# Kernel optimization log

Measured on AMD Instinct MI355X. Metric: run time of the kernel, lower is better.

The kernel has to match this reference:

```python
import jax, jax.numpy as jnp
import numpy as np
from jax import lax

H_IMG, W_IMG = 1280, 1280
STRIDES = (8, 16, 32, 64, 128)
FEAT_SHAPES = tuple((H_IMG // s) * (W_IMG // s) for s in STRIDES)  # (25600,6400,1600,400,100)
N_POINTS = sum(FEAT_SHAPES)  # 34100
NUM_CLASSES = 1
TOPK = 1000
SCORE_THRESH = 0.05
NMS_THRESH = 0.5
MAX_DET = 300
BATCH = 8
N_GT = 200


def make_points():
    # matches AnchorFreePS.reference_points: cell centers at stride*i + stride//2, (cx, cy) order
    pts = []
    for s in STRIDES:
        h, w = H_IMG // s, W_IMG // s
        cx = np.arange(w, dtype=np.float32) * s + s // 2
        cy = np.arange(h, dtype=np.float32) * s + s // 2
        gy, gx = np.meshgrid(cy, cx, indexing='ij')
        pts.append(np.stack([gx, gy], axis=-1).reshape(-1, 2))
    return jnp.asarray(np.concatenate(pts, axis=0))


def setup_inputs() -> dict:
    key = jax.random.key(0)
    k1, k2, k3, k4 = jax.random.split(key, 4)
    points = make_points()  # [N,2]
    xy = jax.random.uniform(k1, (BATCH, N_GT, 2), minval=0.0, maxval=1000.0)
    wh = jax.random.uniform(k2, (BATCH, N_GT, 2), minval=20.0, maxval=260.0)
    gt_boxes = jnp.concatenate([xy, xy + wh], axis=-1)  # [B,M,4] x1y1x2y2
    cls_logits = jax.random.normal(k3, (BATCH, N_POINTS, NUM_CLASSES)) * 1.5 - 3.0
    regression = jax.random.uniform(k4, (BATCH, N_POINTS, 4)) * 0.1  # normalized ltrb codes
    return {"points": points, "gt_boxes": gt_boxes, "cls_logits": cls_logits, "regression": regression}


def match_points_to_boxes(points, gt_boxes):
    # point-in-box test + area-cost argmin (compute_loss matched_idxs)
    px = points[None, :, None, 0]  # [1,N,1]
    py = points[None, :, None, 1]
    b = gt_boxes[:, None, :, :]    # [B,1,M,4]
    inside = (px >= b[..., 0]) & (px <= b[..., 2]) & (py >= b[..., 1]) & (py <= b[..., 3])  # [B,N,M]
    matched = jnp.any(inside, axis=-1)  # [B,N]
    areas = (gt_boxes[..., 2] - gt_boxes[..., 0]) * (gt_boxes[..., 3] - gt_boxes[..., 1])  # [B,M]
    BIG = jnp.float32(2 ** 31 - 1)  # torch.iinfo(torch.int).max
    cost = jnp.where(inside, areas[:, None, :], BIG)
    idx = jnp.argmin(cost, axis=-1)
    return jnp.where(matched, idx, -1)


def decode_boxes(rel, pts):
    # FCOSBoxCoder.decode_single with weights (1,1,1,1)
    l = rel[:, 0] * W_IMG
    t = rel[:, 1] * H_IMG
    r = rel[:, 2] * W_IMG
    b = rel[:, 3] * H_IMG
    x, y = pts[:, 0], pts[:, 1]
    return jnp.stack([x - l, y - t, x + r, y + b], axis=-1)


def clip_boxes(boxes):
    return jnp.stack([
        jnp.clip(boxes[:, 0], 0.0, W_IMG),
        jnp.clip(boxes[:, 1], 0.0, H_IMG),
        jnp.clip(boxes[:, 2], 0.0, W_IMG),
        jnp.clip(boxes[:, 3], 0.0, H_IMG)], axis=-1)


def nms(boxes, scores, labels, valid_init):
    # fixed-size sequential NMS equivalent to batched_nms (same-label suppression)
    work = lax.stop_gradient(jnp.where(valid_init, scores, -jnp.inf))

    def body(w, _):
        i = jnp.argmax(w)
        s = w[i]
        box = boxes[i]
        x1 = jnp.maximum(box[0], boxes[:, 0])
        y1 = jnp.maximum(box[1], boxes[:, 1])
        x2 = jnp.minimum(box[2], boxes[:, 2])
        y2 = jnp.minimum(box[3], boxes[:, 3])
        inter = jnp.clip(x2 - x1, 0.0) * jnp.clip(y2 - y1, 0.0)
        a1 = (box[2] - box[0]) * (box[3] - box[1])
        a2 = (boxes[:, 2] - boxes[:, 0]) * (boxes[:, 3] - boxes[:, 1])
        iou = inter / (a1 + a2 - inter + 1e-9)
        supp = (iou > NMS_THRESH) & (labels == labels[i])
        w = jnp.where(supp, -jnp.inf, w).at[i].set(-jnp.inf)
        return w, (i, s)

    _, (idxs, picked) = lax.scan(body, work, None, length=MAX_DET)
    valid = picked > -jnp.inf
    return idxs, valid


def postprocess_image(points, cls_i, reg_i):
    bx_list, sc_list, lb_list = [], [], []
    off = 0
    for size in FEAT_SHAPES:  # fixed small level loop
        sl = slice(off, off + size)
        off += size
        scores = jax.nn.sigmoid(cls_i[sl]).reshape(-1)  # [size*C]
        k = min(TOPK, size * NUM_CLASSES)
        sc, idx = lax.top_k(scores, k)
        a = idx // NUM_CLASSES
        lb = idx % NUM_CLASSES
        bx = clip_boxes(decode_boxes(reg_i[sl][a], points[sl][a]))
        bx_list.append(bx)
        sc_list.append(sc)
        lb_list.append(lb)
    boxes = jnp.concatenate(bx_list, axis=0)
    scores = jnp.concatenate(sc_list, axis=0)
    labels = jnp.concatenate(lb_list, axis=0)
    idxs, valid = nms(boxes, scores, labels, scores > SCORE_THRESH)
    out_boxes = jnp.where(valid[:, None], boxes[idxs], 0.0)
    out_scores = jnp.where(valid, scores[idxs], 0.0)
    out_labels = jnp.where(valid, labels[idxs], -1)
    return out_boxes, out_scores, out_labels, valid


def reference(points, gt_boxes, cls_logits, regression):
    matched_idxs = match_points_to_boxes(points, gt_boxes)  # [B,N]
    boxes, scores, labels, valid = jax.vmap(
        lambda c, r: postprocess_image(points, c, r))(cls_logits, regression)
    return matched_idxs, boxes, scores, labels, valid
```

## Files before the change

kernel.cpp:

```cpp
#include <hip/hip_runtime.h>
#include <stdint.h>

#define N_POINTS   34100
#define BATCH      8
#define N_GT       200
#define NLEV       5
#define NCAND      3500
#define MAX_DET    300
#define SCORE_TH   0.05f
#define NMS_TH     0.5f
#define IMG        1280.0f
#define NBIN       4096
#define TIE_CAP    4096
#define MTH 0.50000002980232238769531250

#define OUT_MATCH  0
#define OUT_BOXES  272800
#define OUT_SCORES 282400
#define OUT_LABELS 284800
#define OUT_VALID  287200

#define WS_KEYS    0
#define WS_SBOX    2632192
#define WS_SSC     3080192
#define WS_MASK    3192192
#define WS_DIAG    9500032
#define MASK_STRIDE 98560
#define DIAG_STRIDE 3520

typedef unsigned long long u64;
typedef uint32_t u32;

__device__ __forceinline__ int mask_off(int c) {
    int g = c >> 6;
    return 64 * (55 * g - (g * (g - 1)) / 2) + (c - (g << 6)) * (55 - g);
}

__device__ __forceinline__ int level_of(int p) {
    return (p < 25600) ? 0 : (p < 32000) ? 1 : (p < 33600) ? 2 : (p < 34000) ? 3 : 4;
}
__device__ __forceinline__ int loff_of(int l) {
    return (l == 0) ? 0 : (l == 1) ? 25600 : (l == 2) ? 32000 : (l == 3) ? 33600 : 34000;
}
__device__ __forceinline__ int k_of(int l) {
    return (l == 0) ? 1000 : (l == 1) ? 1000 : (l == 2) ? 1000 : (l == 3) ? 400 : 100;
}
__device__ __forceinline__ u64 readlane64(u64 v, int t) {
    u32 lo = (u32)__builtin_amdgcn_readlane((int)(u32)v, t);
    u32 hi = (u32)__builtin_amdgcn_readlane((int)(u32)(v >> 32), t);
    return ((u64)hi << 32) | lo;
}

#define MPT 2
__global__ __launch_bounds__(256)
void match_key_kernel(const float* __restrict__ points,
                      const float* __restrict__ gt,
                      const float* __restrict__ logits,
                      float* __restrict__ out_match,
                      u32* __restrict__ keys) {
#pragma clang fp contract(off)
    __shared__ float bx1[N_GT], by1[N_GT], bx2[N_GT], by2[N_GT], ar[N_GT];
    const int b = blockIdx.y;
    const int base = blockIdx.x * (256 * MPT) + threadIdx.x;

    for (int j = threadIdx.x; j < N_GT; j += 256) {
        float x1 = gt[(b * N_GT + j) * 4 + 0];
        float y1 = gt[(b * N_GT + j) * 4 + 1];
        float x2 = gt[(b * N_GT + j) * 4 + 2];
        float y2 = gt[(b * N_GT + j) * 4 + 3];
        bx1[j] = x1; by1[j] = y1; bx2[j] = x2; by2[j] = y2;
        ar[j] = (x2 - x1) * (y2 - y1);
    }
    __syncthreads();

    const float BIGF = 2147483648.0f;
    float px[MPT], py[MPT], best[MPT];
    int bi[MPT];
#pragma unroll
    for (int k = 0; k < MPT; ++k) {
        int p = base + k * 256;
        int pc = (p < N_POINTS) ? p : 0;
        px[k] = points[pc * 2 + 0];
        py[k] = points[pc * 2 + 1];
        best[k] = BIGF; bi[k] = -1;
    }
    for (int j = 0; j < N_GT; ++j) {
        float x1 = bx1[j], y1 = by1[j], x2 = bx2[j], y2 = by2[j], a = ar[j];
#pragma unroll
        for (int k = 0; k < MPT; ++k) {
            bool inside = (px[k] >= x1) && (px[k] <= x2) &&
                          (py[k] >= y1) && (py[k] <= y2);
            float cost = inside ? a : BIGF;
            if (cost < best[k]) { best[k] = cost; bi[k] = j; }
        }
    }
#pragma unroll
    for (int k = 0; k < MPT; ++k) {
        int p = base + k * 256;
        if (p >= N_POINTS) continue;
        out_match[b * N_POINTS + p] = (float)bi[k];
        float lg = logits[b * N_POINTS + p];
        float s = 1.0f / (1.0f + expf(-lg));
        u32 u = __float_as_uint(s);
        u32 key = (u & 0x80000000u) ? ~u : (u | 0x80000000u);
        keys[b * N_POINTS + p] = key;
    }
}

#define SORT_T 1024
__global__ __launch_bounds__(SORT_T)
void pipeline_kernel(const u32* __restrict__ keys,
                     const float* __restrict__ reg,
                     const float* __restrict__ points,
                     float* __restrict__ sboxes,
                     float* __restrict__ sscores) {
#pragma clang fp contract(off)
    __shared__ __align__(16) char smem[131072];
    u64* sk   = (u64*)smem;
    u32* hist = (u32*)(smem + 32768);
    u64* tb   = (u64*)(smem + 32768);
    u64* aux  = (u64*)(smem + 65536);
    u32* h    = (u32*)(smem + 98304);
    u32* bs   = (u32*)(smem + 114688);
    __shared__ u32 sTl[NLEV], skkl[NLEV], wt[16];
    __shared__ u32 scnt, stcnt;

    const int b = blockIdx.x;
    const int tid = threadIdx.x;
    const int lane = tid & 63;
    const int wid = tid >> 6;
    const u32* kk_ = keys + b * N_POINTS;

    for (int i = tid; i < NLEV * NBIN; i += SORT_T) hist[i] = 0u;
    if (tid == 0) { scnt = 0u; stcnt = 0u; }
    __syncthreads();
    for (int i = tid; i < N_POINTS; i += SORT_T) {
        u32 key = kk_[i];
        atomicAdd(&hist[level_of(i) * NBIN + ((key >> 19) & 4095u)], 1u);
    }
    __syncthreads();

    if (wid < NLEV) {
        const u32 K = (u32)k_of(wid);
        const u32* hh = hist + wid * NBIN;
        u32 S = 0;
#pragma unroll 8
        for (int i = 0; i < 64; ++i) S += hh[lane * 64 + i];
        u32 acc = S;
#pragma unroll
        for (int off = 1; off < 64; off <<= 1) {
            u32 v = (u32)__shfl_down((int)acc, off);
            if (lane + off < 64) acc += v;
        }
        u32 sfxAfter = acc - S;
        bool hit = (sfxAfter < K) && (sfxAfter + S >= K);
        u64 bal = __ballot(hit);
        int Lg = (int)__builtin_ctzll(bal);
        u32 sfxG = (u32)__shfl((int)sfxAfter, Lg);

        u32 v = hh[Lg * 64 + lane];
        u32 acc2 = v;
#pragma unroll
        for (int off = 1; off < 64; off <<= 1) {
            u32 t = (u32)__shfl_down((int)acc2, off);
            if (lane + off < 64) acc2 += t;
        }
        u32 sfx2 = sfxG + acc2 - v;
        bool hit2 = (sfx2 < K) && (sfx2 + v >= K);
        if (hit2) { sTl[wid] = (u32)(Lg * 64 + lane); skkl[wid] = K - sfx2; }
    }
    __syncthreads();

    const u64 below = (lane == 0) ? 0ull : (~0ull >> (64 - lane));
    for (int i0 = tid; i0 - tid < N_POINTS; i0 += SORT_T) {
        bool active = i0 < N_POINTS;
        int pc = active ? i0 : (N_POINTS - 1);
        u32 key = kk_[pc];
        int l = level_of(pc);
        u32 digit = (key >> 19) & 4095u;
        u32 T = sTl[l];
        bool isDef = active && (digit > T);
        bool isTie = active && (digit == T);
        u64 k50 = ((u64)key << 18) | ((u64)(7 - l) << 15)
                | (u64)(32767 - (pc - loff_of(l)));
        u64 grp = __ballot(isDef);
        if (grp) {
            int leader = (int)__builtin_ctzll(grp);
            u32 base_ = 0;
            if (lane == leader)
                base_ = atomicAdd(&scnt, (u32)__builtin_popcountll(grp));
            base_ = (u32)__shfl((int)base_, leader);
            if (isDef) sk[base_ + (u32)__builtin_popcountll(grp & below)] = k50;
        }
        u64 tg = __ballot(isTie);
        if (tg) {
            int leader = (int)__builtin_ctzll(tg);
            u32 base_ = 0;
            if (lane == leader)
                base_ = atomicAdd(&stcnt, (u32)__builtin_popcountll(tg));
            base_ = (u32)__shfl((int)base_, leader);
            if (isTie) {
                u32 pos = base_ + (u32)__builtin_popcountll(tg & below);
                if (pos < TIE_CAP) tb[pos] = k50;
            }
        }
    }
    __syncthreads();

    int t = (int)stcnt; if (t > TIE_CAP) t = TIE_CAP;
    for (int j0 = tid; j0 - tid < t; j0 += SORT_T) {
        bool active = j0 < t;
        u64 kj = active ? tb[j0] : 0ull;
        u32 lvtag = (u32)(kj >> 15) & 7u;
        int r = 0;
        for (int i = 0; i < t; ++i) {
            u64 ki = tb[i];
            r += (ki > kj && (((u32)(ki >> 15) & 7u) == lvtag)) ? 1 : 0;
        }
        bool inc = active && (r < (int)skkl[7 - lvtag]);
        u64 grp = __ballot(inc);
        if (grp) {
            int leader = (int)__builtin_ctzll(grp);
            u32 base_ = 0;
            if (lane == leader)
                base_ = atomicAdd(&scnt, (u32)__builtin_popcountll(grp));
            base_ = (u32)__shfl((int)base_, leader);
            if (inc) sk[base_ + (u32)__builtin_popcountll(grp & below)] = kj;
        }
    }
    __syncthreads();
    const int total = (int)scnt;

    for (int i = tid; i < NBIN; i += SORT_T) h[i] = 0u;
    __syncthreads();
    for (int i = tid; i < total; i += SORT_T)
        atomicAdd(&h[(u32)(sk[i] >> 37) & 4095u], 1u);
    __syncthreads();

    u32 t0 = h[4095 - 4 * tid];
    u32 t1 = h[4095 - (4 * tid + 1)];
    u32 t2 = h[4095 - (4 * tid + 2)];
    u32 t3 = h[4095 - (4 * tid + 3)];
    u32 tsum = t0 + t1 + t2 + t3;
    u32 sc_ = tsum;
#pragma unroll
    for (int off = 1; off < 64; off <<= 1) {
        u32 v = (u32)__shfl_up((int)sc_, off);
        if (lane >= off) sc_ += v;
    }
    if (lane == 63) wt[wid] = sc_;
    __syncthreads();
    if (tid < 64) {
        u32 v = (tid < 16) ? wt[tid] : 0u;
        u32 s2 = v;
#pragma unroll
        for (int off = 1; off < 16; off <<= 1) {
            u32 x = (u32)__shfl_up((int)s2, off);
            if (tid >= off) s2 += x;
        }
        if (tid < 16) wt[tid] = s2 - v;
    }
    __syncthreads();
    u32 run = (sc_ - tsum) + wt[wid];
    bs[4095 - 4 * tid] = run;       run += t0;
    bs[4095 - (4 * tid + 1)] = run; run += t1;
    bs[4095 - (4 * tid + 2)] = run; run += t2;
    bs[4095 - (4 * tid + 3)] = run;
    __syncthreads();
    for (int i = tid; i < NBIN; i += SORT_T) h[i] = 0u;
    __syncthreads();
    for (int i = tid; i < total; i += SORT_T) {
        u64 k = sk[i];
        u32 d = (u32)(k >> 37) & 4095u;
        u32 pos = bs[d] + atomicAdd(&h[d], 1u);
        aux[pos] = k;
    }
    __syncthreads();
    for (int p = tid; p < total; p += SORT_T) {
        u64 kp = aux[p];
        u32 d = (u32)(kp >> 37) & 4095u;
        u32 gbase = bs[d];
        u32 gend = (d == 0) ? (u32)total : bs[d - 1];
        u32 r = 0;
        for (u32 q = gbase; q < gend; ++q) r += (aux[q] > kp) ? 1u : 0u;
        sk[gbase + r] = kp;
    }
    __syncthreads();

    for (int r = tid; r < NCAND; r += SORT_T) {
        float x1 = 0.f, y1 = 0.f, x2 = 0.f, y2 = 0.f, sc = 0.f;
        if (r < total) {
            u64 k50 = sk[r];
            int lowb = (int)(k50 & 0x3FFFFull);
            int l = 7 - (lowb >> 15);
            int idxl = 32767 - (lowb & 32767);
            int p = loff_of(l) + idxl;
            u32 key32 = (u32)(k50 >> 18);
            sc = __uint_as_float(key32 ^ 0x80000000u);
            int gp = b * N_POINTS + p;
            float l_ = reg[gp * 4 + 0] * IMG;
            float t_ = reg[gp * 4 + 1] * IMG;
            float r_ = reg[gp * 4 + 2] * IMG;
            float bb = reg[gp * 4 + 3] * IMG;
            float px = points[p * 2 + 0];
            float py = points[p * 2 + 1];
            x1 = fminf(fmaxf(px - l_, 0.0f), IMG);
            y1 = fminf(fmaxf(py - t_, 0.0f), IMG);
            x2 = fminf(fmaxf(px + r_, 0.0f), IMG);
            y2 = fminf(fmaxf(py + bb, 0.0f), IMG);
        }
        int slot = b * NCAND + r;
        sboxes[slot * 4 + 0] = x1;
        sboxes[slot * 4 + 1] = y1;
        sboxes[slot * 4 + 2] = x2;
        sboxes[slot * 4 + 3] = y2;
        sscores[slot] = sc;
    }
}

__global__ __launch_bounds__(256)
void mask_kernel(const float* __restrict__ sboxes,
                 const float* __restrict__ sscores,
                 u64* __restrict__ mask,
                 u64* __restrict__ diag) {
#pragma clang fp contract(off)
    const int b = blockIdx.y;
    const int wv = threadIdx.x >> 6;
    const int lane = threadIdx.x & 63;
    const int NG = (NCAND + 3) >> 2;
    const int NH = (NG + 1) >> 1;
    const int gidx = blockIdx.x * 4 + wv;
    if (gidx >= NH) return;

    const float4* gb = (const float4*)sboxes + b * NCAND;
    const float* gs = sscores + b * NCAND;
    u64* mout = mask + (size_t)b * MASK_STRIDE;
    u64* dout = diag + (size_t)b * DIAG_STRIDE;

    for (int s = 0; s < 2; ++s) {
        const int g0 = (s == 0) ? gidx : (NG - 1 - gidx);
        if (s == 1 && g0 == gidx) break;
        const int c0 = g0 << 2;

        float4 bc[4]; float a1[4]; bool ok[4]; int g[4]; u64* rp[4];
        bool any = false;
#pragma unroll
        for (int i = 0; i < 4; ++i) {
            int c = c0 + i;
            int cc = (c < NCAND) ? c : (NCAND - 1);
            bc[i] = gb[cc];
            a1[i] = (bc[i].z - bc[i].x) * (bc[i].w - bc[i].y);
            ok[i] = (c < NCAND) && (gs[cc] > SCORE_TH);
            g[i] = cc >> 6;
            rp[i] = mout + mask_off(cc) - g[i];
            any |= ok[i];
        }
        if (!any) continue;

        for (int w = (c0 >> 6); w < 55; ++w) {
            int cj = (w << 6) + lane;
            float4 bj = (cj < NCAND) ? gb[cj] : make_float4(0.f, 0.f, 0.f, 0.f);
            float a2 = (bj.z - bj.x) * (bj.w - bj.y);
#pragma unroll
            for (int i = 0; i < 4; ++i) {
                float x1 = fmaxf(bc[i].x, bj.x);
                float y1 = fmaxf(bc[i].y, bj.y);
                float x2 = fminf(bc[i].z, bj.z);
                float y2 = fminf(bc[i].w, bj.w);
                float inter = fmaxf(x2 - x1, 0.f) * fmaxf(y2 - y1, 0.f);
                float denom = a1[i] + a2 - inter + 1e-9f;
                float hf = 0.5f * denom;
                float rr = fmaf(0x1p-25f, denom, hf);
                u64 bits = __ballot(inter > rr);
                u64 eq = __ballot(inter == rr);
                if (eq) {
                    u64 fb = __ballot((double)inter > MTH * (double)denom);
                    bits |= (eq & fb);
                }
                if (lane == 0 && ok[i] && w >= g[i]) {
                    rp[i][w] = bits;
                    if (w == g[i]) dout[c0 + i] = bits;
                }
            }
        }
    }
}

__global__ __launch_bounds__(64)
void scan_kernel(const float* __restrict__ sboxes,
                 const float* __restrict__ sscores,
                 const u64* __restrict__ mask,
                 const u64* __restrict__ diag,
                 float* __restrict__ out) {
    const int b = blockIdx.x;
    const int lane = threadIdx.x;
    const float4* gb = (const float4*)sboxes + b * NCAND;
    const float* gs = sscores + b * NCAND;
    const u64* mrow = mask + (size_t)b * MASK_STRIDE;
    const u64* drow = diag + (size_t)b * DIAG_STRIDE;

    float* ob = out + OUT_BOXES  + b * MAX_DET * 4;
    float* os = out + OUT_SCORES + b * MAX_DET;
    float* ol = out + OUT_LABELS + b * MAX_DET;
    float* ov = out + OUT_VALID  + b * MAX_DET;

    u64 m = 0ull;
    u64 rowN = drow[lane];
    float4 bjN = gb[lane];
    float sjN = gs[lane];

    int kept = 0;
    for (int w = 0; w < 55; ++w) {
        const int wbase = w << 6;
        const u64 row = rowN;
        const float4 bj = bjN;
        const float sj = sjN;
        if (w < 54) {
            int cn = wbase + 64 + lane;
            int cc = (cn < NCAND) ? cn : (NCAND - 1);
            rowN = drow[cc];
            bjN = gb[cc];
            float s = gs[cc];
            sjN = (cn < NCAND) ? s : 0.f;
        }
        int c = wbase + lane;
        u64 bad = __ballot(!((c < NCAND) && (sj > SCORE_TH)));
        u64 cur = readlane64(m, w) | bad;
        u64 km = 0ull;
        while (kept < MAX_DET) {
            u64 avail = ~cur;
            if (avail == 0ull) break;
            int t = (int)__builtin_ctzll(avail);
            u64 r = readlane64(row, t);
            cur |= r | (1ull << t);
            km |= 1ull << t;
            if (lane == t) {
                ob[kept * 4 + 0] = bj.x;
                ob[kept * 4 + 1] = bj.y;
                ob[kept * 4 + 2] = bj.z;
                ob[kept * 4 + 3] = bj.w;
                os[kept] = sj;
                ol[kept] = 0.0f;
                ov[kept] = 1.0f;
            }
            kept++;
        }
        if (km) {
            const bool lr = (lane >= w && lane < 55);
            const int lo = lane - w;
            u64 acc = 0ull;
            while (km) {
#define POPBIT(tn) int tn = -1; if (km) { tn = (int)__builtin_ctzll(km); km &= km - 1ull; }
                POPBIT(t0) POPBIT(t1) POPBIT(t2) POPBIT(t3)
                POPBIT(t4) POPBIT(t5) POPBIT(t6) POPBIT(t7)
#undef POPBIT
                u64 v0 = 0, v1 = 0, v2 = 0, v3 = 0, v4 = 0, v5 = 0, v6 = 0, v7 = 0;
                if (lr) {
                    v0 = mrow[mask_off(wbase + t0) + lo];
                    if (t1 >= 0) v1 = mrow[mask_off(wbase + t1) + lo];
                    if (t2 >= 0) v2 = mrow[mask_off(wbase + t2) + lo];
                    if (t3 >= 0) v3 = mrow[mask_off(wbase + t3) + lo];
                    if (t4 >= 0) v4 = mrow[mask_off(wbase + t4) + lo];
                    if (t5 >= 0) v5 = mrow[mask_off(wbase + t5) + lo];
                    if (t6 >= 0) v6 = mrow[mask_off(wbase + t6) + lo];
                    if (t7 >= 0) v7 = mrow[mask_off(wbase + t7) + lo];
                }
                acc |= ((v0 | v1) | (v2 | v3)) | ((v4 | v5) | (v6 | v7));
            }
            m |= acc;
        }
        if (kept >= MAX_DET) break;
    }
    for (int k = kept + lane; k < MAX_DET; k += 64) {
        ob[k * 4 + 0] = 0.f; ob[k * 4 + 1] = 0.f;
        ob[k * 4 + 2] = 0.f; ob[k * 4 + 3] = 0.f;
        os[k] = 0.f; ol[k] = -1.f; ov[k] = 0.f;
    }
}

extern "C" void kernel_launch(void* const* d_in, const int* in_sizes, int n_in,
                              void* d_out, int out_size, void* d_ws, size_t ws_size,
                              hipStream_t stream) {
    const float* points = (const float*)d_in[0];
    const float* gt     = (const float*)d_in[1];
    const float* logits = (const float*)d_in[2];
    const float* reg    = (const float*)d_in[3];
    float* out = (float*)d_out;

    u32* keys      = (u32*)((char*)d_ws + WS_KEYS);
    float* sboxes  = (float*)((char*)d_ws + WS_SBOX);
    float* sscores = (float*)((char*)d_ws + WS_SSC);
    u64* mask   = (u64*)((char*)d_ws + WS_MASK);
    u64* diag   = (u64*)((char*)d_ws + WS_DIAG);

    dim3 g1((N_POINTS + 256 * MPT - 1) / (256 * MPT), BATCH);
    match_key_kernel<<<g1, 256, 0, stream>>>(points, gt, logits,
                                             out + OUT_MATCH, keys);

    pipeline_kernel<<<BATCH, SORT_T, 0, stream>>>(keys, reg, points,
                                                  sboxes, sscores);

    dim3 g5((((NCAND + 3) / 4 + 1) / 2 + 3) / 4, BATCH);
    mask_kernel<<<g5, 256, 0, stream>>>(sboxes, sscores, mask, diag);

    scan_kernel<<<BATCH, 64, 0, stream>>>(sboxes, sscores, mask, diag, out);
}
```

Before: 263.9 us.

## Split histogram threshold selection into separate per-level kernel, pair-wise compaction

Moves the per-level histogram and top-k threshold search out of the single-block-per-image pipeline kernel into a new kernel launched with one block per (image, level), writing thresholds to workspace. The compaction pass now handles two points per thread and uses a wave prefix scan with one atomic per wave instead of ballot-based leader atomics. This spreads the histogram work over many more blocks than the eight used before, at the cost of an extra launch and a small global round-trip for the parameters.

New measurement: 280.6 us. 6.4% more time.

```diff
diff --git a/kernel.cpp b/kernel.cpp
--- a/kernel.cpp
+++ b/kernel.cpp
@@ -21,6 +21,7 @@
 #define OUT_VALID  287200
 
 #define WS_KEYS    0
+#define WS_PARAMS  1746560
 #define WS_SBOX    2632192
 #define WS_SSC     3080192
 #define WS_MASK    3192192
@@ -41,6 +42,9 @@
 }
 __device__ __forceinline__ int loff_of(int l) {
     return (l == 0) ? 0 : (l == 1) ? 25600 : (l == 2) ? 32000 : (l == 3) ? 33600 : 34000;
+}
+__device__ __forceinline__ int lsize_of(int l) {
+    return (l == 0) ? 25600 : (l == 1) ? 6400 : (l == 2) ? 1600 : (l == 3) ? 400 : 100;
 }
 __device__ __forceinline__ int k_of(int l) {
     return (l == 0) ? 1000 : (l == 1) ? 1000 : (l == 2) ? 1000 : (l == 3) ? 400 : 100;
@@ -107,21 +111,72 @@
     }
 }
 
+__global__ __launch_bounds__(256)
+void hist_select_kernel(const u32* __restrict__ keys,
+                        u32* __restrict__ params) {
+    __shared__ u32 h[NBIN];
+    const int seg = blockIdx.x;
+    const int b = seg / NLEV;
+    const int l = seg - b * NLEV;
+    const int tid = threadIdx.x;
+
+    for (int i = tid; i < NBIN; i += 256) h[i] = 0u;
+    __syncthreads();
+
+    const u32* k = keys + b * N_POINTS + loff_of(l);
+    const int n = lsize_of(l);
+    for (int i = tid; i < n; i += 256)
+        atomicAdd(&h[(k[i] >> 19) & 4095u], 1u);
+    __syncthreads();
+
+    if (tid < 64) {
+        const u32 K = (u32)k_of(l);
+        const int lane = tid;
+        u32 S = 0;
+#pragma unroll 8
+        for (int i = 0; i < 64; ++i) S += h[lane * 64 + i];
+        u32 acc = S;
+#pragma unroll
+        for (int off = 1; off < 64; off <<= 1) {
+            u32 v = (u32)__shfl_down((int)acc, off);
+            if (lane + off < 64) acc += v;
+        }
+        u32 sfxAfter = acc - S;
+        bool hit = (sfxAfter < K) && (sfxAfter + S >= K);
+        u64 bal = __ballot(hit);
+        int Lg = (int)__builtin_ctzll(bal);
+        u32 sfxG = (u32)__shfl((int)sfxAfter, Lg);
+
+        u32 v = h[Lg * 64 + lane];
+        u32 acc2 = v;
+#pragma unroll
+        for (int off = 1; off < 64; off <<= 1) {
+            u32 t = (u32)__shfl_down((int)acc2, off);
+            if (lane + off < 64) acc2 += t;
+        }
+        u32 sfx2 = sfxG + acc2 - v;
+        bool hit2 = (sfx2 < K) && (sfx2 + v >= K);
+        if (hit2) {
+            params[seg * 2 + 0] = (u32)(Lg * 64 + lane);
+            params[seg * 2 + 1] = K - sfx2;
+        }
+    }
+}
+
 #define SORT_T 1024
 __global__ __launch_bounds__(SORT_T)
 void pipeline_kernel(const u32* __restrict__ keys,
+                     const u32* __restrict__ params,
                      const float* __restrict__ reg,
                      const float* __restrict__ points,
                      float* __restrict__ sboxes,
                      float* __restrict__ sscores) {
 #pragma clang fp contract(off)
-    __shared__ __align__(16) char smem[131072];
-    u64* sk   = (u64*)smem;
-    u32* hist = (u32*)(smem + 32768);
-    u64* tb   = (u64*)(smem + 32768);
-    u64* aux  = (u64*)(smem + 65536);
-    u32* h    = (u32*)(smem + 98304);
-    u32* bs   = (u32*)(smem + 114688);
+    __shared__ u64 sk[4096];
+    __shared__ u64 tb[TIE_CAP];
+    __shared__ u64 aux[4096];
+    __shared__ u32 h[NBIN];
+    __shared__ u32 bs[NBIN];
     __shared__ u32 sTl[NLEV], skkl[NLEV], wt[16];
     __shared__ u32 scnt, stcnt;
 
@@ -131,82 +186,61 @@
     const int wid = tid >> 6;
     const u32* kk_ = keys + b * N_POINTS;
 
-    for (int i = tid; i < NLEV * NBIN; i += SORT_T) hist[i] = 0u;
+    if (tid < NLEV) {
+        sTl[tid]  = params[(b * NLEV + tid) * 2 + 0];
+        skkl[tid] = params[(b * NLEV + tid) * 2 + 1];
+    }
     if (tid == 0) { scnt = 0u; stcnt = 0u; }
     __syncthreads();
-    for (int i = tid; i < N_POINTS; i += SORT_T) {
-        u32 key = kk_[i];
-        atomicAdd(&hist[level_of(i) * NBIN + ((key >> 19) & 4095u)], 1u);
-    }
-    __syncthreads();
-
-    if (wid < NLEV) {
-        const u32 K = (u32)k_of(wid);
-        const u32* hh = hist + wid * NBIN;
-        u32 S = 0;
-#pragma unroll 8
-        for (int i = 0; i < 64; ++i) S += hh[lane * 64 + i];
-        u32 acc = S;
+
+    const int NPAIR = N_POINTS / 2;
+    for (int i0 = tid; i0 - tid < NPAIR; i0 += SORT_T) {
+        bool act = i0 < NPAIR;
+        int p0 = act ? (2 * i0) : 0;
+        int p1 = p0 + 1;
+        u32 key0 = kk_[p0], key1 = kk_[p1];
+        int l0 = level_of(p0), l1 = level_of(p1);
+        u32 d0 = (key0 >> 19) & 4095u, d1 = (key1 >> 19) & 4095u;
+        u32 T0 = sTl[l0], T1 = sTl[l1];
+        bool def0 = act && (d0 > T0), def1 = act && (d1 > T1);
+        bool tie0 = act && (d0 == T0), tie1 = act && (d1 == T1);
+        u64 k0 = ((u64)key0 << 18) | ((u64)(7 - l0) << 15)
+               | (u64)(32767 - (p0 - loff_of(l0)));
+        u64 k1 = ((u64)key1 << 18) | ((u64)(7 - l1) << 15)
+               | (u64)(32767 - (p1 - loff_of(l1)));
+
+        u32 nd = (u32)def0 + (u32)def1;
+        u32 pre = nd;
 #pragma unroll
         for (int off = 1; off < 64; off <<= 1) {
-            u32 v = (u32)__shfl_down((int)acc, off);
-            if (lane + off < 64) acc += v;
-        }
-        u32 sfxAfter = acc - S;
-        bool hit = (sfxAfter < K) && (sfxAfter + S >= K);
-        u64 bal = __ballot(hit);
-        int Lg = (int)__builtin_ctzll(bal);
-        u32 sfxG = (u32)__shfl((int)sfxAfter, Lg);
-
-        u32 v = hh[Lg * 64 + lane];
-        u32 acc2 = v;
+            u32 v = (u32)__shfl_up((int)pre, off);
+            if (lane >= off) pre += v;
+        }
+        u32 base_ = 0;
+        if (lane == 63 && pre) base_ = atomicAdd(&scnt, pre);
+        base_ = (u32)__shfl((int)base_, 63);
+        u32 ex = pre - nd;
+        if (def0) sk[base_ + ex] = k0;
+        if (def1) sk[base_ + ex + (u32)def0] = k1;
+
+        u32 nt = (u32)tie0 + (u32)tie1;
+        u32 pret = nt;
 #pragma unroll
         for (int off = 1; off < 64; off <<= 1) {
-            u32 t = (u32)__shfl_down((int)acc2, off);
-            if (lane + off < 64) acc2 += t;
-        }
-        u32 sfx2 = sfxG + acc2 - v;
-        bool hit2 = (sfx2 < K) && (sfx2 + v >= K);
-        if (hit2) { sTl[wid] = (u32)(Lg * 64 + lane); skkl[wid] = K - sfx2; }
+            u32 v = (u32)__shfl_up((int)pret, off);
+            if (lane >= off) pret += v;
+        }
+        u32 baset = 0;
+        if (lane == 63 && pret) baset = atomicAdd(&stcnt, pret);
+        baset = (u32)__shfl((int)baset, 63);
+        u32 ext = pret - nt;
+        if (tie0 && baset + ext < TIE_CAP) tb[baset + ext] = k0;
+        if (tie1 && baset + ext + (u32)tie0 < TIE_CAP)
+            tb[baset + ext + (u32)tie0] = k1;
     }
     __syncthreads();
 
     const u64 below = (lane == 0) ? 0ull : (~0ull >> (64 - lane));
-    for (int i0 = tid; i0 - tid < N_POINTS; i0 += SORT_T) {
-        bool active = i0 < N_POINTS;
-        int pc = active ? i0 : (N_POINTS - 1);
-        u32 key = kk_[pc];
-        int l = level_of(pc);
-        u32 digit = (key >> 19) & 4095u;
-        u32 T = sTl[l];
-        bool isDef = active && (digit > T);
-        bool isTie = active && (digit == T);
-        u64 k50 = ((u64)key << 18) | ((u64)(7 - l) << 15)
-                | (u64)(32767 - (pc - loff_of(l)));
-        u64 grp = __ballot(isDef);
-        if (grp) {
-            int leader = (int)__builtin_ctzll(grp);
-            u32 base_ = 0;
-            if (lane == leader)
-                base_ = atomicAdd(&scnt, (u32)__builtin_popcountll(grp));
-            base_ = (u32)__shfl((int)base_, leader);
-            if (isDef) sk[base_ + (u32)__builtin_popcountll(grp & below)] = k50;
-        }
-        u64 tg = __ballot(isTie);
-        if (tg) {
-            int leader = (int)__builtin_ctzll(tg);
-            u32 base_ = 0;
-            if (lane == leader)
-                base_ = atomicAdd(&stcnt, (u32)__builtin_popcountll(tg));
-            base_ = (u32)__shfl((int)base_, leader);
-            if (isTie) {
-                u32 pos = base_ + (u32)__builtin_popcountll(tg & below);
-                if (pos < TIE_CAP) tb[pos] = k50;
-            }
-        }
-    }
-    __syncthreads();
-
     int t = (int)stcnt; if (t > TIE_CAP) t = TIE_CAP;
     for (int j0 = tid; j0 - tid < t; j0 += SORT_T) {
         bool active = j0 < t;
@@ -488,6 +522,7 @@
     float* out = (float*)d_out;
 
     u32* keys      = (u32*)((char*)d_ws + WS_KEYS);
+    u32* params    = (u32*)((char*)d_ws + WS_PARAMS);
     float* sboxes  = (float*)((char*)d_ws + WS_SBOX);
     float* sscores = (float*)((char*)d_ws + WS_SSC);
     u64* mask   = (u64*)((char*)d_ws + WS_MASK);
@@ -497,7 +532,9 @@
     match_key_kernel<<<g1, 256, 0, stream>>>(points, gt, logits,
                                              out + OUT_MATCH, keys);
 
-    pipeline_kernel<<<BATCH, SORT_T, 0, stream>>>(keys, reg, points,
+    hist_select_kernel<<<BATCH * NLEV, 256, 0, stream>>>(keys, params);
+
+    pipeline_kernel<<<BATCH, SORT_T, 0, stream>>>(keys, params, reg, points,
                                                   sboxes, sscores);
 
     dim3 g5((((NCAND + 3) / 4 + 1) / 2 + 3) / 4, BATCH);
```
